# Optimization experiments

Measured on AMD Instinct MI355X. Metric: run time of the kernel, lower is better.

## Reference

```python
import jax, jax.numpy as jnp
import numpy as np

NUM_BITS = 8
QMIN = -(2.0 ** (NUM_BITS - 1)) + 1.0   # -127
QMAX = 2.0 ** (NUM_BITS - 1) - 1.0      # 127
RUN_MIN, RUN_MAX = -1.0, 1.0            # eval-mode running_min/running_max buffers
KERNEL, STRIDE, PAD = 3, 1, 1

# input scale (concrete, from running stats): scale = max(|min|,|max|)/qmax, snapped to power of 2
_scale_in = max(max(abs(RUN_MAX), abs(RUN_MIN)) / QMAX, 1e-8)
INPUT_SCALE = float(2.0 ** np.round(np.log2(_scale_in)))  # 2^-7


def _ste_quant(x, scale):
    """shift (x/scale), clamp to [QMIN,QMAX], round; straight-through grad = 1/scale."""
    xs = x / scale
    return xs + jax.lax.stop_gradient(jnp.round(jnp.clip(xs, QMIN, QMAX)) - xs)


def _weight_scale(w):
    s = jnp.maximum(jnp.maximum(jnp.abs(jnp.max(w)), jnp.abs(jnp.min(w))) / QMAX, 1e-8)
    return 2.0 ** jnp.round(jnp.log2(s))


def _adder2d(qx, qw):
    """AdderNet SAD conv: out[n,f,i,j] = -sum_{c,kh,kw} |patch - w|."""
    N = qx.shape[0]
    Cout = qw.shape[0]
    patches = jax.lax.conv_general_dilated_patches(
        qx, (KERNEL, KERNEL), (STRIDE, STRIDE), [(PAD, PAD), (PAD, PAD)])
    _, K, Ho, Wo = patches.shape            # K = Cin*k*k, channel-major like OIHW reshape
    pr = patches.reshape(N, K, Ho * Wo)
    wf = qw.reshape(Cout, K)

    def per_out(wk):                         # wk: [K]
        return -jnp.sum(jnp.abs(pr - wk[None, :, None]), axis=1)  # [N, Ho*Wo]

    out = jax.lax.map(jax.checkpoint(per_out), wf)   # [Cout, N, Ho*Wo], sequential over Cout
    return jnp.transpose(out, (1, 0, 2)).reshape(N, Cout, Ho, Wo)


def reference(x, weight):
    # quantize input (eval mode, running stats scale = 2^-7)
    qx = _ste_quant(x, INPUT_SCALE)
    # quantize weight at its own power-of-2 scale (scale_index < 0 branch)
    s_w = jax.lax.stop_gradient(_weight_scale(weight))
    qw = _ste_quant(weight, s_w)
    # integer-domain SAD convolution
    q_out = _adder2d(qx, qw)
    # dequantize: round, clamp to int32 range, shift right by |scale_index| (== * INPUT_SCALE);
    # straight-through grad = INPUT_SCALE
    ys = q_out * INPUT_SCALE
    deq = jnp.clip(jnp.round(q_out), -2.0 ** 31 + 1, 2.0 ** 31 - 1) * INPUT_SCALE
    return ys + jax.lax.stop_gradient(deq - ys)


def setup_inputs() -> dict:
    key = jax.random.key(0)
    kx, kw = jax.random.split(key)
    x = jax.random.normal(kx, (16, 32, 128, 128), dtype=jnp.float32)
    weight = jax.random.normal(kw, (32, 32, 3, 3), dtype=jnp.float32)
    return {"x": x, "weight": weight}
```

## Files before the change

kernel.cpp:

```cpp
#include <hip/hip_runtime.h>
#include <stdint.h>

#define INPUT_SCALE 0.0078125f

__device__ __forceinline__ uint32_t sadu8(uint32_t a, uint32_t b, uint32_t c) {
#if __has_builtin(__builtin_amdgcn_sad_u8)
    return __builtin_amdgcn_sad_u8(a, b, c);
#else
    uint32_t d;
    asm("v_sad_u8 %0, %1, %2, %3" : "=v"(d) : "v"(a), "v"(b), "v"(c));
    return d;
#endif
}

__device__ __forceinline__ uint32_t qbyte(float x) {
    float v = fminf(fmaxf(x * 128.0f, -127.0f), 127.0f);
    return (uint32_t)((int)rintf(v) + 128);
}

__global__ __launch_bounds__(1024) void quant_weight(const float* __restrict__ w,
                                                     uint32_t* __restrict__ qwp) {
    __shared__ float red[1024];
    __shared__ float s_inv;
    int tid = threadIdx.x;
    float m = 0.0f;
    for (int i = tid; i < 9216; i += 1024) m = fmaxf(m, fabsf(w[i]));
    red[tid] = m;
    __syncthreads();
    for (int s = 512; s > 0; s >>= 1) {
        if (tid < s) red[tid] = fmaxf(red[tid], red[tid + s]);
        __syncthreads();
    }
    if (tid == 0) {
        float s = fmaxf(red[0] / 127.0f, 1e-8f);
        int e; float fr = frexpf(s, &e);
        int k = (fr >= 0.70710678118654752f) ? e : e - 1;
        s_inv = exp2f((float)(-k));
    }
    __syncthreads();
    float inv = s_inv;
    for (int u = tid; u < 2304; u += 1024) {
        int t = u >> 8;
        int rem = u & 255;
        int f = rem >> 3, cg = rem & 7;
        int kh = t / 3, kw = t - kh * 3;
        uint32_t pk = 0;
        #pragma unroll
        for (int b = 0; b < 4; ++b) {
            int c = cg * 4 + b;
            float v = w[((f * 32 + c) * 3 + kh) * 3 + kw] * inv;
            v = fminf(fmaxf(v, -127.0f), 127.0f);
            pk |= ((uint32_t)((int)rintf(v) + 128) & 0xFFu) << (8 * b);
        }
        qwp[u] = pk;
    }
}

#define LSTRIDE 12
__global__ __launch_bounds__(512, 8) void adder_conv_fused(const float* __restrict__ x,
                                                           const uint32_t* __restrict__ qwp,
                                                           float* __restrict__ out) {
    __shared__ __align__(16) uint32_t sx[10 * 34 * LSTRIDE];
    int tid = threadIdx.x;
    int b = ((blockIdx.x & 7) << 7) + (blockIdx.x >> 3);
    int n = b >> 6;
    int rem = b & 63;
    int h0 = (rem >> 2) * 8, w0 = (rem & 3) * 32;

    for (int q = tid; q < 2720; q += 512) {
        int cg = q / 340;
        int pixel = q - cg * 340;
        int r = pixel / 34, cc = pixel - r * 34;
        int gh = h0 - 1 + r, gw = w0 - 1 + cc;
        uint32_t pk = 0x80808080u;
        if ((unsigned)gh < 128u && (unsigned)gw < 128u) {
            const float* base = x + (((size_t)n * 32 + cg * 4) * 128 + gh) * 128 + gw;
            pk = qbyte(base[0])
               | (qbyte(base[16384]) << 8)
               | (qbyte(base[32768]) << 16)
               | (qbyte(base[49152]) << 24);
        }
        sx[pixel * LSTRIDE + cg] = pk;
    }
    __syncthreads();

    int fh = __builtin_amdgcn_readfirstlane(tid >> 8);
    int px = tid & 255;
    int r = px >> 5;
    int c = px & 31;

    uint32_t acc[16];
    #pragma unroll
    for (int f = 0; f < 16; ++f) acc[f] = 0u;

    int lbase = (r * 34 + c) * LSTRIDE;
    #pragma unroll 1
    for (int kh = 0; kh < 3; ++kh) {
        #pragma unroll 1
        for (int kw = 0; kw < 3; ++kw) {
            const uint4* p = (const uint4*)(sx + lbase + (kh * 34 + kw) * LSTRIDE);
            uint4 x0 = p[0];
            uint4 x1 = p[1];
            const uint32_t* wt = qwp + (((kh * 3 + kw) * 32) + fh * 16) * 8;
            #pragma unroll
            for (int f = 0; f < 16; ++f) {
                const uint4* wp = (const uint4*)(wt + f * 8);
                uint4 wv0 = wp[0], wv1 = wp[1];
                uint32_t a = acc[f];
                a = sadu8(x0.x, wv0.x, a);
                a = sadu8(x0.y, wv0.y, a);
                a = sadu8(x0.z, wv0.z, a);
                a = sadu8(x0.w, wv0.w, a);
                a = sadu8(x1.x, wv1.x, a);
                a = sadu8(x1.y, wv1.y, a);
                a = sadu8(x1.z, wv1.z, a);
                a = sadu8(x1.w, wv1.w, a);
                acc[f] = a;
            }
        }
    }

    size_t obase = (((size_t)n * 32 + fh * 16) * 128 + (h0 + r)) * 128 + (w0 + c);
    #pragma unroll
    for (int f = 0; f < 16; ++f) {
        out[obase + (size_t)f * 16384] = -(float)acc[f] * INPUT_SCALE;
    }
}

extern "C" void kernel_launch(void* const* d_in, const int* in_sizes, int n_in,
                              void* d_out, int out_size, void* d_ws, size_t ws_size,
                              hipStream_t stream) {
    const float* x = (const float*)d_in[0];
    const float* w = (const float*)d_in[1];
    float* out = (float*)d_out;

    uint32_t* qwp = (uint32_t*)d_ws;

    quant_weight<<<1, 1024, 0, stream>>>(w, qwp);
    adder_conv_fused<<<1024, 512, 0, stream>>>(x, qwp, out);
}
```

Measured before the change: 39.81 us.

## Pre-quantize input into padded packed global buffer, drop LDS staging in conv

```diff
diff --git a/kernel.cpp b/kernel.cpp
--- a/kernel.cpp
+++ b/kernel.cpp
@@ -18,11 +18,30 @@
     return (uint32_t)((int)rintf(v) + 128);
 }
 
-__global__ __launch_bounds__(1024) void quant_weight(const float* __restrict__ w,
-                                                     uint32_t* __restrict__ qwp) {
+#define PIMG 16900
+#define PROW 130
+
+__global__ __launch_bounds__(1024) void quant_weight_border(const float* __restrict__ w,
+                                                            uint32_t* __restrict__ qwp,
+                                                            uint32_t* __restrict__ qxp) {
+    int tid = threadIdx.x;
+    if (blockIdx.x != 0) {
+        int idx = (blockIdx.x - 1) * 1024 + tid;
+        if (idx < 16 * 516) {
+            int n = idx / 516, i = idx - n * 516;
+            int r, c;
+            if (i < 130)      { r = 0;   c = i; }
+            else if (i < 260) { r = 129; c = i - 130; }
+            else if (i < 388) { r = 1 + (i - 260); c = 0; }
+            else              { r = 1 + (i - 388); c = 129; }
+            uint4* p = (uint4*)(qxp + ((size_t)n * PIMG + r * PROW + c) * 8);
+            uint4 v = make_uint4(0x80808080u, 0x80808080u, 0x80808080u, 0x80808080u);
+            p[0] = v; p[1] = v;
+        }
+        return;
+    }
     __shared__ float red[1024];
     __shared__ float s_inv;
-    int tid = threadIdx.x;
     float m = 0.0f;
     for (int i = tid; i < 9216; i += 1024) m = fmaxf(m, fabsf(w[i]));
     red[tid] = m;
@@ -56,52 +75,67 @@
     }
 }
 
-#define LSTRIDE 12
-__global__ __launch_bounds__(512, 8) void adder_conv_fused(const float* __restrict__ x,
-                                                           const uint32_t* __restrict__ qwp,
-                                                           float* __restrict__ out) {
-    __shared__ __align__(16) uint32_t sx[10 * 34 * LSTRIDE];
+__global__ __launch_bounds__(256) void quant_pack_x(const float4* __restrict__ x4,
+                                                    uint4* __restrict__ qxp4) {
+    int t = blockIdx.x * blockDim.x + threadIdx.x;
+    int n = t >> 12;
+    int rem = t & 4095;
+    int h = rem >> 5;
+    int wg = rem & 31;
+    uint32_t pk[4][8];
+    #pragma unroll
+    for (int pix = 0; pix < 4; ++pix)
+        #pragma unroll
+        for (int cg = 0; cg < 8; ++cg) pk[pix][cg] = 0u;
+    #pragma unroll
+    for (int c = 0; c < 32; ++c) {
+        float4 v = x4[((size_t)(n * 32 + c) * 128 + h) * 32 + wg];
+        int cg = c >> 2, sh = (c & 3) << 3;
+        pk[0][cg] |= qbyte(v.x) << sh;
+        pk[1][cg] |= qbyte(v.y) << sh;
+        pk[2][cg] |= qbyte(v.z) << sh;
+        pk[3][cg] |= qbyte(v.w) << sh;
+    }
+    size_t base = ((size_t)n * PIMG + (h + 1) * PROW + (wg * 4 + 1)) * 2;
+    #pragma unroll
+    for (int pix = 0; pix < 4; ++pix) {
+        qxp4[base + pix * 2 + 0] = make_uint4(pk[pix][0], pk[pix][1], pk[pix][2], pk[pix][3]);
+        qxp4[base + pix * 2 + 1] = make_uint4(pk[pix][4], pk[pix][5], pk[pix][6], pk[pix][7]);
+    }
+}
+
+__global__ __launch_bounds__(512, 8) void adder_conv(const uint32_t* __restrict__ qxp,
+                                                     const uint32_t* __restrict__ qwp,
+                                                     float* __restrict__ out) {
     int tid = threadIdx.x;
     int b = ((blockIdx.x & 7) << 7) + (blockIdx.x >> 3);
     int n = b >> 6;
     int rem = b & 63;
     int h0 = (rem >> 2) * 8, w0 = (rem & 3) * 32;
 
-    for (int q = tid; q < 2720; q += 512) {
-        int cg = q / 340;
-        int pixel = q - cg * 340;
-        int r = pixel / 34, cc = pixel - r * 34;
-        int gh = h0 - 1 + r, gw = w0 - 1 + cc;
-        uint32_t pk = 0x80808080u;
-        if ((unsigned)gh < 128u && (unsigned)gw < 128u) {
-            const float* base = x + (((size_t)n * 32 + cg * 4) * 128 + gh) * 128 + gw;
-            pk = qbyte(base[0])
-               | (qbyte(base[16384]) << 8)
-               | (qbyte(base[32768]) << 16)
-               | (qbyte(base[49152]) << 24);
-        }
-        sx[pixel * LSTRIDE + cg] = pk;
-    }
-    __syncthreads();
-
     int fh = __builtin_amdgcn_readfirstlane(tid >> 8);
     int px = tid & 255;
     int r = px >> 5;
     int c = px & 31;
+    int gh = h0 + r, gw = w0 + c;
+
+    const char* bbase = (const char*)qxp + ((size_t)n * PIMG + gh * PROW + gw) * 32;
 
     uint32_t acc[16];
     #pragma unroll
     for (int f = 0; f < 16; ++f) acc[f] = 0u;
 
-    int lbase = (r * 34 + c) * LSTRIDE;
     #pragma unroll 1
     for (int kh = 0; kh < 3; ++kh) {
-        #pragma unroll 1
+        const uint4* rp = (const uint4*)(bbase + kh * (PROW * 32));
+        uint4 p00 = rp[0], p01 = rp[1];
+        uint4 p10 = rp[2], p11 = rp[3];
+        uint4 p20 = rp[4], p21 = rp[5];
+        #pragma unroll
         for (int kw = 0; kw < 3; ++kw) {
-            const uint4* p = (const uint4*)(sx + lbase + (kh * 34 + kw) * LSTRIDE);
-            uint4 x0 = p[0];
-            uint4 x1 = p[1];
-            const uint32_t* wt = qwp + (((kh * 3 + kw) * 32) + fh * 16) * 8;
+            uint4 x0 = (kw == 0) ? p00 : (kw == 1) ? p10 : p20;
+            uint4 x1 = (kw == 0) ? p01 : (kw == 1) ? p11 : p21;
+            const uint32_t* wt = qwp + ((kh * 3 + kw) * 32 + fh * 16) * 8;
             #pragma unroll
             for (int f = 0; f < 16; ++f) {
                 const uint4* wp = (const uint4*)(wt + f * 8);
@@ -120,7 +154,7 @@
         }
     }
 
-    size_t obase = (((size_t)n * 32 + fh * 16) * 128 + (h0 + r)) * 128 + (w0 + c);
+    size_t obase = (((size_t)n * 32 + fh * 16) * 128 + gh) * 128 + gw;
     #pragma unroll
     for (int f = 0; f < 16; ++f) {
         out[obase + (size_t)f * 16384] = -(float)acc[f] * INPUT_SCALE;
@@ -135,7 +169,9 @@
     float* out = (float*)d_out;
 
     uint32_t* qwp = (uint32_t*)d_ws;
+    uint32_t* qxp = (uint32_t*)((char*)d_ws + 16384);
 
-    quant_weight<<<1, 1024, 0, stream>>>(w, qwp);
-    adder_conv_fused<<<1024, 512, 0, stream>>>(x, qwp, out);
+    quant_weight_border<<<10, 1024, 0, stream>>>(w, qwp, qxp);
+    quant_pack_x<<<256, 256, 0, stream>>>((const float4*)x, (uint4*)qxp);
+    adder_conv<<<1024, 512, 0, stream>>>(qxp, qwp, out);
 }
```

Measured after the change: 45.12 us. 1.13x slower.

## Compute two output rows per thread and split weight quantization across blocks

Applied to the files above, without the earlier changes.

```diff
diff --git a/kernel.cpp b/kernel.cpp
--- a/kernel.cpp
+++ b/kernel.cpp
@@ -18,16 +18,16 @@
     return (uint32_t)((int)rintf(v) + 128);
 }
 
-__global__ __launch_bounds__(1024) void quant_weight(const float* __restrict__ w,
-                                                     uint32_t* __restrict__ qwp) {
-    __shared__ float red[1024];
+__global__ __launch_bounds__(256) void quant_weight(const float* __restrict__ w,
+                                                    uint32_t* __restrict__ qwp) {
+    __shared__ float red[256];
     __shared__ float s_inv;
     int tid = threadIdx.x;
     float m = 0.0f;
-    for (int i = tid; i < 9216; i += 1024) m = fmaxf(m, fabsf(w[i]));
+    for (int i = tid; i < 9216; i += 256) m = fmaxf(m, fabsf(w[i]));
     red[tid] = m;
     __syncthreads();
-    for (int s = 512; s > 0; s >>= 1) {
+    for (int s = 128; s > 0; s >>= 1) {
         if (tid < s) red[tid] = fmaxf(red[tid], red[tid + s]);
         __syncthreads();
     }
@@ -39,7 +39,8 @@
     }
     __syncthreads();
     float inv = s_inv;
-    for (int u = tid; u < 2304; u += 1024) {
+    int u = blockIdx.x * 256 + tid;
+    {
         int t = u >> 8;
         int rem = u & 255;
         int f = rem >> 3, cg = rem & 7;
@@ -57,7 +58,7 @@
 }
 
 #define LSTRIDE 12
-__global__ __launch_bounds__(512, 8) void adder_conv_fused(const float* __restrict__ x,
+__global__ __launch_bounds__(256, 4) void adder_conv_fused(const float* __restrict__ x,
                                                            const uint32_t* __restrict__ qwp,
                                                            float* __restrict__ out) {
     __shared__ __align__(16) uint32_t sx[10 * 34 * LSTRIDE];
@@ -67,7 +68,7 @@
     int rem = b & 63;
     int h0 = (rem >> 2) * 8, w0 = (rem & 3) * 32;
 
-    for (int q = tid; q < 2720; q += 512) {
+    for (int q = tid; q < 2720; q += 256) {
         int cg = q / 340;
         int pixel = q - cg * 340;
         int r = pixel / 34, cc = pixel - r * 34;
@@ -84,38 +85,53 @@
     }
     __syncthreads();
 
-    int fh = __builtin_amdgcn_readfirstlane(tid >> 8);
-    int px = tid & 255;
-    int r = px >> 5;
-    int c = px & 31;
+    int fh = __builtin_amdgcn_readfirstlane(tid >> 7);
+    int p = tid & 127;
+    int r = p >> 5;
+    int c = p & 31;
 
-    uint32_t acc[16];
+    uint32_t acc[2][16];
     #pragma unroll
-    for (int f = 0; f < 16; ++f) acc[f] = 0u;
+    for (int j = 0; j < 2; ++j)
+        #pragma unroll
+        for (int f = 0; f < 16; ++f) acc[j][f] = 0u;
 
-    int lbase = (r * 34 + c) * LSTRIDE;
+    int lb0 = (r * 34 + c) * LSTRIDE;
+    int lb1 = ((r + 4) * 34 + c) * LSTRIDE;
     #pragma unroll 1
     for (int kh = 0; kh < 3; ++kh) {
         #pragma unroll 1
         for (int kw = 0; kw < 3; ++kw) {
-            const uint4* p = (const uint4*)(sx + lbase + (kh * 34 + kw) * LSTRIDE);
-            uint4 x0 = p[0];
-            uint4 x1 = p[1];
-            const uint32_t* wt = qwp + (((kh * 3 + kw) * 32) + fh * 16) * 8;
+            int toff = (kh * 34 + kw) * LSTRIDE;
+            const uint4* p0 = (const uint4*)(sx + lb0 + toff);
+            const uint4* p1 = (const uint4*)(sx + lb1 + toff);
+            uint4 a0 = p0[0], a1 = p0[1];
+            uint4 b0 = p1[0], b1 = p1[1];
+            const uint32_t* wt = qwp + ((kh * 3 + kw) * 32 + fh * 16) * 8;
             #pragma unroll
             for (int f = 0; f < 16; ++f) {
                 const uint4* wp = (const uint4*)(wt + f * 8);
                 uint4 wv0 = wp[0], wv1 = wp[1];
-                uint32_t a = acc[f];
-                a = sadu8(x0.x, wv0.x, a);
-                a = sadu8(x0.y, wv0.y, a);
-                a = sadu8(x0.z, wv0.z, a);
-                a = sadu8(x0.w, wv0.w, a);
-                a = sadu8(x1.x, wv1.x, a);
-                a = sadu8(x1.y, wv1.y, a);
-                a = sadu8(x1.z, wv1.z, a);
-                a = sadu8(x1.w, wv1.w, a);
-                acc[f] = a;
+                uint32_t s = acc[0][f];
+                s = sadu8(a0.x, wv0.x, s);
+                s = sadu8(a0.y, wv0.y, s);
+                s = sadu8(a0.z, wv0.z, s);
+                s = sadu8(a0.w, wv0.w, s);
+                s = sadu8(a1.x, wv1.x, s);
+                s = sadu8(a1.y, wv1.y, s);
+                s = sadu8(a1.z, wv1.z, s);
+                s = sadu8(a1.w, wv1.w, s);
+                acc[0][f] = s;
+                uint32_t t2 = acc[1][f];
+                t2 = sadu8(b0.x, wv0.x, t2);
+                t2 = sadu8(b0.y, wv0.y, t2);
+                t2 = sadu8(b0.z, wv0.z, t2);
+                t2 = sadu8(b0.w, wv0.w, t2);
+                t2 = sadu8(b1.x, wv1.x, t2);
+                t2 = sadu8(b1.y, wv1.y, t2);
+                t2 = sadu8(b1.z, wv1.z, t2);
+                t2 = sadu8(b1.w, wv1.w, t2);
+                acc[1][f] = t2;
             }
         }
     }
@@ -123,7 +139,8 @@
     size_t obase = (((size_t)n * 32 + fh * 16) * 128 + (h0 + r)) * 128 + (w0 + c);
     #pragma unroll
     for (int f = 0; f < 16; ++f) {
-        out[obase + (size_t)f * 16384] = -(float)acc[f] * INPUT_SCALE;
+        out[obase + (size_t)f * 16384]       = -(float)acc[0][f] * INPUT_SCALE;
+        out[obase + (size_t)f * 16384 + 512] = -(float)acc[1][f] * INPUT_SCALE;
     }
 }
 
@@ -136,6 +153,6 @@
 
     uint32_t* qwp = (uint32_t*)d_ws;
 
-    quant_weight<<<1, 1024, 0, stream>>>(w, qwp);
-    adder_conv_fused<<<1024, 512, 0, stream>>>(x, qwp, out);
+    quant_weight<<<9, 256, 0, stream>>>(w, qwp);
+    adder_conv_fused<<<1024, 256, 0, stream>>>(x, qwp, out);
 }
```

Result: slower. 43.84 us (+10.1%).
